# Performance work log

Hardware: AMD Instinct MI355X
Metric: run time of the kernel (lower is better)

## Reference

```python
import jax, jax.numpy as jnp
import numpy as np

N_NODES = 100000
N_EDGES = 1600000
DIM = 128
N_GRAPHS = 64
N_LAYERS = 7
LEAKY_SLOPE = 0.01
BN_EPS = 1e-5


def setup_inputs() -> dict:
    key = jax.random.key(0)
    ks = jax.random.split(key, 6)
    x = jax.random.normal(ks[0], (N_NODES, DIM), dtype=jnp.float32)
    edge_index = jax.random.randint(ks[1], (2, N_EDGES), 0, N_NODES, dtype=jnp.int64)
    batch = jnp.sort(jax.random.randint(ks[2], (N_NODES,), 0, N_GRAPHS, dtype=jnp.int64))
    # GCNConv weights (Glorot-ish scale), biases, BatchNorm affine params
    Ws = jax.random.normal(ks[3], (N_LAYERS, DIM, DIM), dtype=jnp.float32) * (1.0 / np.sqrt(DIM))
    bs = jnp.zeros((N_LAYERS, DIM), dtype=jnp.float32)
    gammas = jnp.ones((N_LAYERS, DIM), dtype=jnp.float32)
    betas = jnp.zeros((N_LAYERS, DIM), dtype=jnp.float32)
    return {"x": x, "edge_index": edge_index, "batch": batch,
            "Ws": Ws, "bs": bs, "gammas": gammas, "betas": betas}


def reference(x, edge_index, batch, Ws, bs, gammas, betas):
    N = x.shape[0]
    # Add self-loops once (shared by all 7 GCNConv layers)
    loops = jnp.arange(N, dtype=edge_index.dtype)
    src = jnp.concatenate([edge_index[0], loops])  # [E+N]
    dst = jnp.concatenate([edge_index[1], loops])  # [E+N]
    # Symmetric normalization: deg over destination (incl. self-loops)
    deg = jax.ops.segment_sum(jnp.ones_like(dst, dtype=x.dtype), dst, num_segments=N)
    dinv = jax.lax.rsqrt(jnp.maximum(deg, 1.0))  # deg >= 1 from self-loops
    norm = dinv[src] * dinv[dst]                 # [E+N]

    def block(h, W, b, gamma, beta):
        # GCNConv: linear -> gather -> normalized scatter-add
        h = h @ W + b                                            # [N, D]
        msgs = h[src] * norm[:, None]                            # [E+N, D]
        h = jax.ops.segment_sum(msgs, dst, num_segments=N)       # [N, D]
        # LeakyReLU then BatchNorm (batch statistics over nodes)
        h = jax.nn.leaky_relu(h, negative_slope=LEAKY_SLOPE)
        mu = jnp.mean(h, axis=0)
        var = jnp.mean((h - mu) ** 2, axis=0)
        h = (h - mu) * jax.lax.rsqrt(var + BN_EPS) * gamma + beta
        return h

    h = x
    for i in range(N_LAYERS):
        h = block(h, Ws[i], bs[i], gammas[i], betas[i])

    # global_mean_pool over graph ids
    sums = jax.ops.segment_sum(h, batch, num_segments=N_GRAPHS)          # [G, D]
    cnt = jax.ops.segment_sum(jnp.ones((N,), h.dtype), batch, num_segments=N_GRAPHS)
    return sums / jnp.maximum(cnt, 1.0)[:, None]
```

## Files before the change

kernel.cpp:

```cpp
#include <hip/hip_runtime.h>
#include <hip/hip_fp16.h>

#define DIMM 128
#define LEAKY_S 0.01f
#define EPS_BN 1e-5f

typedef _Float16 half8 __attribute__((ext_vector_type(8)));
typedef float f32x4 __attribute__((ext_vector_type(4)));


__global__ __launch_bounds__(256) void k_deg(const int* __restrict__ dst, int* __restrict__ deg, int E, int N) {
    int i = blockIdx.x * 256 + threadIdx.x;
    if (i < E) {
        int d = dst[i];
        if ((unsigned)d < (unsigned)N) atomicAdd(&deg[d], 1);
    }
}

__global__ __launch_bounds__(256) void k_dinv(const int* __restrict__ deg, float* __restrict__ dinv, int N) {
    int i = blockIdx.x * 256 + threadIdx.x;
    if (i < N) dinv[i] = rsqrtf((float)(deg[i] + 1));
}

__global__ __launch_bounds__(256) void k_scanA(const int* __restrict__ deg, int* __restrict__ bsum, int n) {
    __shared__ int ws[4];
    int tid = threadIdx.x, lane = tid & 63, wid = tid >> 6;
    int base = blockIdx.x * 1024;
    int s = 0;
    #pragma unroll
    for (int j = 0; j < 4; ++j) {
        int i = base + j * 256 + tid;
        if (i < n) s += deg[i];
    }
    #pragma unroll
    for (int off = 32; off > 0; off >>= 1) s += __shfl_down(s, (unsigned)off, 64);
    if (lane == 0) ws[wid] = s;
    __syncthreads();
    if (tid == 0) bsum[blockIdx.x] = ws[0] + ws[1] + ws[2] + ws[3];
}

__global__ __launch_bounds__(64) void k_scanB(const int* __restrict__ bsum, int* __restrict__ bofs,
                                              int* __restrict__ rowptr, int nb, int n) {
    if (threadIdx.x == 0) {
        int run = 0;
        for (int j = 0; j < nb; ++j) { bofs[j] = run; run += bsum[j]; }
        rowptr[n] = run;
    }
}

__global__ __launch_bounds__(1024) void k_scanC(const int* __restrict__ deg, const int* __restrict__ bofs,
                                                int* __restrict__ rowptr, int n) {
    __shared__ int wsum[16];
    int tid = threadIdx.x, lane = tid & 63, wid = tid >> 6;
    int i = blockIdx.x * 1024 + tid;
    int v = (i < n) ? deg[i] : 0;
    int s = v;
    #pragma unroll
    for (int off = 1; off < 64; off <<= 1) {
        int t = __shfl_up(s, (unsigned)off, 64);
        if (lane >= off) s += t;
    }
    if (lane == 63) wsum[wid] = s;
    __syncthreads();
    if (wid == 0 && lane < 16) {
        int ws = wsum[lane];
        #pragma unroll
        for (int off = 1; off < 16; off <<= 1) {
            int t = __shfl_up(ws, (unsigned)off, 64);
            if (lane >= off) ws += t;
        }
        wsum[lane] = ws;
    }
    __syncthreads();
    int woff = wid ? wsum[wid - 1] : 0;
    if (i < n) rowptr[i] = bofs[blockIdx.x] + woff + (s - v);
}

__global__ __launch_bounds__(256) void k_fill(const int* __restrict__ src, const int* __restrict__ dst,
                                              const int* __restrict__ rowptr, int* __restrict__ cursor,
                                              const float* __restrict__ dinv,
                                              int2* __restrict__ csr, int E, int N) {
    int i = blockIdx.x * 256 + threadIdx.x;
    if (i < E) {
        int d = dst[i], s = src[i];
        if ((unsigned)d < (unsigned)N && (unsigned)s < (unsigned)N) {
            int pos = atomicAdd(&cursor[d], 1);
            int idx = rowptr[d] + pos;
            csr[idx] = make_int2(s, __float_as_int(dinv[s] * dinv[d]));
        }
    }
}


__global__ __launch_bounds__(256) void k_wprep(const float* __restrict__ Ws, __half* __restrict__ Wt) {
    int l = blockIdx.y;
    int i = blockIdx.x * 256 + threadIdx.x;
    int n = i >> 7, k = i & 127;
    Wt[(size_t)l * DIMM * DIMM + n * DIMM + k] = __float2half(Ws[(size_t)l * DIMM * DIMM + k * DIMM + n]);
}


__global__ __launch_bounds__(256) void k_gemm(const void* __restrict__ A, const __half* __restrict__ Wt,
                                              const float* __restrict__ bias, const float* __restrict__ ss,
                                              __half* __restrict__ out, int N, int a_half) {
    __shared__ char smem[128 * 272];
    int tid = threadIdx.x;
    int lane = tid & 63, wid = tid >> 6;
    int quad = lane >> 4, lm = lane & 15;
    int row0 = blockIdx.x * 128;

    {
        int seg = tid & 31;
        int col = seg * 4;
        float4 sc = *(const float4*)(ss + col);
        float4 sh = *(const float4*)(ss + 128 + col);
        const float*  Af = (const float*)A;
        const __half* Ah = (const __half*)A;
        for (int i = tid; i < 128 * 32; i += 256) {
            int r = i >> 5;
            int gr = row0 + r;
            float4 v = make_float4(0.f, 0.f, 0.f, 0.f);
            if (gr < N) {
                if (a_half) {
                    union { uint2 u; __half2 h2[2]; } ld;
                    ld.u = *(const uint2*)(Ah + (size_t)gr * DIMM + col);
                    float2 f0 = __half22float2(ld.h2[0]);
                    float2 f1 = __half22float2(ld.h2[1]);
                    v = make_float4(f0.x, f0.y, f1.x, f1.y);
                } else {
                    v = *(const float4*)(Af + (size_t)gr * DIMM + col);
                }
                v.x = v.x * sc.x + sh.x; v.y = v.y * sc.y + sh.y;
                v.z = v.z * sc.z + sh.z; v.w = v.w * sc.w + sh.w;
            }
            union { _Float16 h[4]; uint2 u; } pk;
            pk.h[0] = (_Float16)v.x; pk.h[1] = (_Float16)v.y;
            pk.h[2] = (_Float16)v.z; pk.h[3] = (_Float16)v.w;
            *(uint2*)(smem + r * 272 + seg * 8) = pk.u;
        }
    }

    f32x4 acc[2][8];
    #pragma unroll
    for (int c = 0; c < 8; ++c) {
        float bc = bias[c * 16 + lm];
        acc[0][c] = (f32x4){bc, bc, bc, bc};
        acc[1][c] = acc[0][c];
    }
    __syncthreads();

    const _Float16* Wt16 = (const _Float16*)Wt;
    #pragma unroll
    for (int kc = 0; kc < 4; ++kc) {
        half8 a0 = *(const half8*)(smem + (wid * 32 + lm) * 272 + kc * 64 + quad * 16);
        half8 a1 = *(const half8*)(smem + (wid * 32 + 16 + lm) * 272 + kc * 64 + quad * 16);
        #pragma unroll
        for (int c = 0; c < 8; ++c) {
            half8 b = *(const half8*)(Wt16 + (c * 16 + lm) * DIMM + kc * 32 + quad * 8);
            acc[0][c] = __builtin_amdgcn_mfma_f32_16x16x32_f16(a0, b, acc[0][c], 0, 0, 0);
            acc[1][c] = __builtin_amdgcn_mfma_f32_16x16x32_f16(a1, b, acc[1][c], 0, 0, 0);
        }
    }

    __syncthreads();
    #pragma unroll
    for (int r = 0; r < 2; ++r)
        #pragma unroll
        for (int c = 0; c < 8; ++c)
            #pragma unroll
            for (int i = 0; i < 4; ++i) {
                int rit = wid * 32 + r * 16 + quad * 4 + i;
                int col = c * 16 + lm;
                *(_Float16*)(smem + rit * 256 + col * 2) = (_Float16)acc[r][c][i];
            }
    __syncthreads();
    for (int i = tid; i < 128 * 16; i += 256) {
        int r = i >> 4, seg = i & 15;
        int gr = row0 + r;
        if (gr < N)
            ((uint4*)(out + (size_t)gr * DIMM))[seg] = ((const uint4*)(smem + r * 256))[seg];
    }
}


__global__ __launch_bounds__(256) void k_agg(const __half* __restrict__ t, __half* __restrict__ out,
                                             const int* __restrict__ rowptr, const int2* __restrict__ csr,
                                             const float* __restrict__ dinv,
                                             float* __restrict__ stats, int N, int nwaves) {
    int tid = threadIdx.x;
    int lane = tid & 63, wid = tid >> 6;
    int grp = lane >> 4;
    int l16 = lane & 15;
    int gw = blockIdx.x * 4 + wid;

    float sx[8] = {0.f, 0.f, 0.f, 0.f, 0.f, 0.f, 0.f, 0.f};
    float qx[8] = {0.f, 0.f, 0.f, 0.f, 0.f, 0.f, 0.f, 0.f};

    int node = gw;
    int e0 = 0, e1 = 0;
    float di = 0.f;
    if (node < N) { e0 = rowptr[node]; e1 = rowptr[node + 1]; di = dinv[node]; }

    while (node < N) {
        int nxt = node + nwaves;
        int ep0 = 0, ep1 = 0;
        float dip = 0.f;
        if (nxt < N) { ep0 = rowptr[nxt]; ep1 = rowptr[nxt + 1]; dip = dinv[nxt]; }

        union { half8 h; __half2 h2[4]; } us;
        us.h = *(const half8*)(t + ((size_t)(unsigned)node << 7) + l16 * 8);

        float v[8] = {0.f, 0.f, 0.f, 0.f, 0.f, 0.f, 0.f, 0.f};

        for (int e = e0; e < e1; e += 32) {
            int2 c[8];
            int last = e1 - 1;
            #pragma unroll
            for (int j = 0; j < 8; ++j) {
                int idx = e + 4 * j + grp;
                int idxc = idx < last ? idx : last;
                c[j] = csr[idxc];
                if (idx >= e1) c[j].y = 0;
            }
            #pragma unroll
            for (int j = 0; j < 8; ++j) {
                float wgt = __int_as_float(c[j].y);
                union { half8 h; __half2 h2[4]; } g;
                g.h = *(const half8*)(t + ((size_t)(unsigned)c[j].x << 7) + l16 * 8);
                #pragma unroll
                for (int p = 0; p < 4; ++p) {
                    float2 f = __half22float2(g.h2[p]);
                    v[2 * p]     = fmaf(wgt, f.x, v[2 * p]);
                    v[2 * p + 1] = fmaf(wgt, f.y, v[2 * p + 1]);
                }
            }
        }

        float sn = (grp == 0) ? di * di : 0.f;
        #pragma unroll
        for (int p = 0; p < 4; ++p) {
            float2 f = __half22float2(us.h2[p]);
            v[2 * p]     = fmaf(sn, f.x, v[2 * p]);
            v[2 * p + 1] = fmaf(sn, f.y, v[2 * p + 1]);
        }

        #pragma unroll
        for (int i = 0; i < 8; ++i) {
            v[i] += __shfl_down(v[i], 32, 64);
            v[i] += __shfl_down(v[i], 16, 64);
        }
        if (grp == 0) {
            union { _Float16 h[8]; uint4 u4; } pk;
            #pragma unroll
            for (int i = 0; i < 8; ++i) {
                v[i] = v[i] > 0.f ? v[i] : LEAKY_S * v[i];
                sx[i] += v[i];
                qx[i] += v[i] * v[i];
                pk.h[i] = (_Float16)v[i];
            }
            *(uint4*)(out + ((size_t)(unsigned)node << 7) + l16 * 8) = pk.u4;
        }

        node = nxt; e0 = ep0; e1 = ep1; di = dip;
    }

    __shared__ float red[4 * 128];
    if (grp == 0) {
        *(float4*)(red + wid * 128 + l16 * 8)     = make_float4(sx[0], sx[1], sx[2], sx[3]);
        *(float4*)(red + wid * 128 + l16 * 8 + 4) = make_float4(sx[4], sx[5], sx[6], sx[7]);
    }
    __syncthreads();
    if (tid < 128) {
        float s = red[tid] + red[128 + tid] + red[256 + tid] + red[384 + tid];
        atomicAdd(&stats[tid], s);
    }
    __syncthreads();
    if (grp == 0) {
        *(float4*)(red + wid * 128 + l16 * 8)     = make_float4(qx[0], qx[1], qx[2], qx[3]);
        *(float4*)(red + wid * 128 + l16 * 8 + 4) = make_float4(qx[4], qx[5], qx[6], qx[7]);
    }
    __syncthreads();
    if (tid < 128) {
        float s = red[tid] + red[128 + tid] + red[256 + tid] + red[384 + tid];
        atomicAdd(&stats[128 + tid], s);
    }
}

__global__ __launch_bounds__(128) void k_bnfin(const float* __restrict__ stats, const float* __restrict__ gamma,
                                               const float* __restrict__ beta, float* __restrict__ ss_out,
                                               float inv_n) {
    int c = threadIdx.x;
    float mu  = stats[c] * inv_n;
    float var = stats[128 + c] * inv_n - mu * mu;
    float a = gamma[c] * rsqrtf(var + EPS_BN);
    ss_out[c]       = a;
    ss_out[128 + c] = beta[c] - mu * a;
}

__global__ __launch_bounds__(128) void k_init_ss(float* __restrict__ ss) {
    int c = threadIdx.x;
    ss[c] = 1.0f;
    ss[128 + c] = 0.0f;
}


__global__ __launch_bounds__(64) void k_cnt_bs(const int* __restrict__ batch, int* __restrict__ cnt, int N, int G) {
    int g = blockIdx.x * 64 + threadIdx.x;
    if (g >= G) return;
    int lo = 0, hi = N;
    while (lo < hi) { int mid = (lo + hi) >> 1; if (batch[mid] < g) lo = mid + 1; else hi = mid; }
    int lb = lo;
    lo = 0; hi = N;
    while (lo < hi) { int mid = (lo + hi) >> 1; if (batch[mid] <= g) lo = mid + 1; else hi = mid; }
    cnt[g] = lo - lb;
}

__global__ __launch_bounds__(128) void k_pool(const __half* __restrict__ h, const int* __restrict__ batch,
                                              float* __restrict__ pool, int N, int G) {
    const int CHUNK = 128;
    int start = blockIdx.x * CHUNK;
    if (start >= N) return;
    int end = min(start + CHUNK, N);
    int tid = threadIdx.x;
    float acc = 0.f;
    int cur = batch[start];
    for (int n = start; n < end; ++n) {
        int g = batch[n];
        if (g != cur) {
            if ((unsigned)cur < (unsigned)G) atomicAdd(&pool[(size_t)cur * DIMM + tid], acc);
            acc = 0.f; cur = g;
        }
        acc += __half2float(h[(size_t)n * DIMM + tid]);
    }
    if ((unsigned)cur < (unsigned)G) atomicAdd(&pool[(size_t)cur * DIMM + tid], acc);
}

__global__ __launch_bounds__(256) void k_poolfin(const float* __restrict__ pool, const int* __restrict__ cnt,
                                                 const float* __restrict__ ss, float* __restrict__ out, int G) {
    int idx = blockIdx.x * 256 + threadIdx.x;
    if (idx < G * DIMM) {
        int g = idx >> 7, c = idx & 127;
        float m = pool[idx] / (float)max(cnt[g], 1);
        out[idx] = ss[c] * m + ss[128 + c];
    }
}


extern "C" void kernel_launch(void* const* d_in, const int* in_sizes, int n_in,
                              void* d_out, int out_size, void* d_ws, size_t ws_size,
                              hipStream_t stream) {
    const float* x      = (const float*)d_in[0];
    const int*   ei     = (const int*)d_in[1];
    const int*   batch  = (const int*)d_in[2];
    const float* Ws     = (const float*)d_in[3];
    const float* bs     = (const float*)d_in[4];
    const float* gammas = (const float*)d_in[5];
    const float* betas  = (const float*)d_in[6];
    float* outp = (float*)d_out;

    int N = in_sizes[2];
    int E = in_sizes[1] / 2;
    int L = in_sizes[3] / (DIMM * DIMM);
    int G = out_size / DIMM;

    const int* srcv = ei;
    const int* dstv = ei + E;

    int nb = (N + 1023) / 1024;

    char* w = (char*)d_ws;
    auto alloc = [&](size_t bytes) { char* p = w; w += (bytes + 511) & ~size_t(511); return p; };
    int*    deg    = (int*)   alloc((size_t)N * 4);
    int*    cursor = (int*)   alloc((size_t)N * 4);
    int*    rowptr = (int*)   alloc((size_t)(N + 1) * 4);
    int*    bsum   = (int*)   alloc((size_t)nb * 4);
    int*    bofs   = (int*)   alloc((size_t)nb * 4);
    int2*   csr    = (int2*)  alloc((size_t)E * 8);
    float*  dinv   = (float*) alloc((size_t)N * 4);
    __half* hA     = (__half*)alloc((size_t)N * DIMM * 2);
    __half* hB     = (__half*)alloc((size_t)N * DIMM * 2);
    __half* Wt     = (__half*)alloc((size_t)L * DIMM * DIMM * 2);
    float*  stats  = (float*) alloc((size_t)L * 256 * 4);
    float*  ss     = (float*) alloc((size_t)(L + 1) * 256 * 4);
    float*  pool   = (float*) alloc((size_t)G * DIMM * 4);
    int*    cnt    = (int*)   alloc((size_t)G * 4);

    hipMemsetAsync(deg,    0, (size_t)N * 4, stream);
    hipMemsetAsync(cursor, 0, (size_t)N * 4, stream);
    hipMemsetAsync(stats,  0, (size_t)L * 256 * 4, stream);
    hipMemsetAsync(pool,   0, (size_t)G * DIMM * 4, stream);

    k_init_ss<<<1, 128, 0, stream>>>(ss);
    k_wprep<<<dim3(64, L), 256, 0, stream>>>(Ws, Wt);
    k_deg  <<<(E + 255) / 256, 256, 0, stream>>>(dstv, deg, E, N);
    k_dinv <<<(N + 255) / 256, 256, 0, stream>>>(deg, dinv, N);
    k_scanA<<<nb, 256, 0, stream>>>(deg, bsum, N);
    k_scanB<<<1, 64, 0, stream>>>(bsum, bofs, rowptr, nb, N);
    k_scanC<<<nb, 1024, 0, stream>>>(deg, bofs, rowptr, N);
    k_fill <<<(E + 255) / 256, 256, 0, stream>>>(srcv, dstv, rowptr, cursor, dinv, csr, E, N);

    const void* cur_in = (const void*)x;
    int a_half = 0;
    for (int l = 0; l < L; ++l) {
        k_gemm<<<(N + 127) / 128, 256, 0, stream>>>(cur_in, Wt + (size_t)l * DIMM * DIMM,
                                                    bs + (size_t)l * DIMM, ss + (size_t)l * 256, hA, N, a_half);
        const int nblk = 2048;
        k_agg<<<nblk, 256, 0, stream>>>(hA, hB, rowptr, csr, dinv,
                                        stats + (size_t)l * 256, N, nblk * 4);
        k_bnfin<<<1, 128, 0, stream>>>(stats + (size_t)l * 256, gammas + (size_t)l * DIMM,
                                       betas + (size_t)l * DIMM, ss + (size_t)(l + 1) * 256, 1.0f / (float)N);
        cur_in = (const void*)hB;
        a_half = 1;
    }

    k_cnt_bs<<<(G + 63) / 64, 64, 0, stream>>>(batch, cnt, N, G);
    k_pool<<<(N + 127) / 128, 128, 0, stream>>>(hB, batch, pool, N, G);
    k_poolfin<<<(G * DIMM + 255) / 256, 256, 0, stream>>>(pool, cnt, ss + (size_t)L * 256, outp, G);
}
```

Before: 1.177 ms.

## Fold BN finalize into GEMM prologue and prefetch next node's CSR edges in aggregation

Drops the separate k_bnfin and k_init_ss launches. Each GEMM block now computes the BatchNorm scale and shift from the raw stats in shared memory, and the pool-finish kernel does the same for the last layer. The aggregation kernel prefetches the first 32 CSR entries of the next node while it finishes the current one, to hide edge-list load latency. The cost is redundant BN math in every GEMM block and extra registers held across iterations of the aggregation loop.

```diff
diff --git a/kernel.cpp b/kernel.cpp
--- a/kernel.cpp
+++ b/kernel.cpp
@@ -101,19 +101,35 @@
 
 
 __global__ __launch_bounds__(256) void k_gemm(const void* __restrict__ A, const __half* __restrict__ Wt,
-                                              const float* __restrict__ bias, const float* __restrict__ ss,
-                                              __half* __restrict__ out, int N, int a_half) {
+                                              const float* __restrict__ bias,
+                                              const float* __restrict__ stats, const float* __restrict__ gamma,
+                                              const float* __restrict__ beta,
+                                              __half* __restrict__ out, int N, int a_half, float inv_n) {
     __shared__ char smem[128 * 272];
+    __shared__ float ssm[256];
     int tid = threadIdx.x;
     int lane = tid & 63, wid = tid >> 6;
     int quad = lane >> 4, lm = lane & 15;
     int row0 = blockIdx.x * 128;
 
+    if (a_half && tid < 128) {
+        float mu  = stats[tid] * inv_n;
+        float var = stats[128 + tid] * inv_n - mu * mu;
+        float a = gamma[tid] * rsqrtf(var + EPS_BN);
+        ssm[tid]       = a;
+        ssm[128 + tid] = beta[tid] - mu * a;
+    }
+    __syncthreads();
+
     {
         int seg = tid & 31;
         int col = seg * 4;
-        float4 sc = *(const float4*)(ss + col);
-        float4 sh = *(const float4*)(ss + 128 + col);
+        float4 sc = make_float4(1.f, 1.f, 1.f, 1.f);
+        float4 sh = make_float4(0.f, 0.f, 0.f, 0.f);
+        if (a_half) {
+            sc = *(const float4*)(ssm + col);
+            sh = *(const float4*)(ssm + 128 + col);
+        }
         const float*  Af = (const float*)A;
         const __half* Ah = (const __half*)A;
         for (int i = tid; i < 128 * 32; i += 256) {
@@ -126,12 +142,11 @@
                     ld.u = *(const uint2*)(Ah + (size_t)gr * DIMM + col);
                     float2 f0 = __half22float2(ld.h2[0]);
                     float2 f1 = __half22float2(ld.h2[1]);
-                    v = make_float4(f0.x, f0.y, f1.x, f1.y);
+                    v = make_float4(f0.x * sc.x + sh.x, f0.y * sc.y + sh.y,
+                                    f1.x * sc.z + sh.z, f1.y * sc.w + sh.w);
                 } else {
                     v = *(const float4*)(Af + (size_t)gr * DIMM + col);
                 }
-                v.x = v.x * sc.x + sh.x; v.y = v.y * sc.y + sh.y;
-                v.z = v.z * sc.z + sh.z; v.w = v.w * sc.w + sh.w;
             }
             union { _Float16 h[4]; uint2 u; } pk;
             pk.h[0] = (_Float16)v.x; pk.h[1] = (_Float16)v.y;
@@ -199,7 +214,20 @@
     int node = gw;
     int e0 = 0, e1 = 0;
     float di = 0.f;
-    if (node < N) { e0 = rowptr[node]; e1 = rowptr[node + 1]; di = dinv[node]; }
+    int2 c[8];
+    if (node < N) {
+        e0 = rowptr[node]; e1 = rowptr[node + 1]; di = dinv[node];
+        int last = e1 - 1;
+        #pragma unroll
+        for (int j = 0; j < 8; ++j) {
+            if (e0 + 4 * j < e1) {
+                int idx = e0 + 4 * j + grp;
+                int idxc = idx < last ? idx : last;
+                c[j] = csr[idxc];
+                if (idx >= e1) c[j].y = 0;
+            }
+        }
+    }
 
     while (node < N) {
         int nxt = node + nwaves;
@@ -212,18 +240,9 @@
 
         float v[8] = {0.f, 0.f, 0.f, 0.f, 0.f, 0.f, 0.f, 0.f};
 
-        for (int e = e0; e < e1; e += 32) {
-            int2 c[8];
-            int last = e1 - 1;
-            #pragma unroll
-            for (int j = 0; j < 8; ++j) {
-                int idx = e + 4 * j + grp;
-                int idxc = idx < last ? idx : last;
-                c[j] = csr[idxc];
-                if (idx >= e1) c[j].y = 0;
-            }
-            #pragma unroll
-            for (int j = 0; j < 8; ++j) {
+        #pragma unroll
+        for (int j = 0; j < 8; ++j) {
+            if (e0 + 4 * j < e1) {
                 float wgt = __int_as_float(c[j].y);
                 union { half8 h; __half2 h2[4]; } g;
                 g.h = *(const half8*)(t + ((size_t)(unsigned)c[j].x << 7) + l16 * 8);
@@ -235,6 +254,27 @@
                 }
             }
         }
+        for (int e = e0 + 32; e < e1; e += 32) {
+            int last = e1 - 1;
+            #pragma unroll
+            for (int j = 0; j < 8; ++j) {
+                if (e + 4 * j < e1) {
+                    int idx = e + 4 * j + grp;
+                    int idxc = idx < last ? idx : last;
+                    int2 cw = csr[idxc];
+                    if (idx >= e1) cw.y = 0;
+                    float wgt = __int_as_float(cw.y);
+                    union { half8 h; __half2 h2[4]; } g;
+                    g.h = *(const half8*)(t + ((size_t)(unsigned)cw.x << 7) + l16 * 8);
+                    #pragma unroll
+                    for (int p = 0; p < 4; ++p) {
+                        float2 f = __half22float2(g.h2[p]);
+                        v[2 * p]     = fmaf(wgt, f.x, v[2 * p]);
+                        v[2 * p + 1] = fmaf(wgt, f.y, v[2 * p + 1]);
+                    }
+                }
+            }
+        }
 
         float sn = (grp == 0) ? di * di : 0.f;
         #pragma unroll
@@ -242,6 +282,19 @@
             float2 f = __half22float2(us.h2[p]);
             v[2 * p]     = fmaf(sn, f.x, v[2 * p]);
             v[2 * p + 1] = fmaf(sn, f.y, v[2 * p + 1]);
+        }
+
+        if (nxt < N) {
+            int lastn = ep1 - 1;
+            #pragma unroll
+            for (int j = 0; j < 8; ++j) {
+                if (ep0 + 4 * j < ep1) {
+                    int idx = ep0 + 4 * j + grp;
+                    int idxc = idx < lastn ? idx : lastn;
+                    c[j] = csr[idxc];
+                    if (idx >= ep1) c[j].y = 0;
+                }
+            }
         }
 
         #pragma unroll
@@ -284,23 +337,6 @@
         float s = red[tid] + red[128 + tid] + red[256 + tid] + red[384 + tid];
         atomicAdd(&stats[128 + tid], s);
     }
-}
-
-__global__ __launch_bounds__(128) void k_bnfin(const float* __restrict__ stats, const float* __restrict__ gamma,
-                                               const float* __restrict__ beta, float* __restrict__ ss_out,
-                                               float inv_n) {
-    int c = threadIdx.x;
-    float mu  = stats[c] * inv_n;
-    float var = stats[128 + c] * inv_n - mu * mu;
-    float a = gamma[c] * rsqrtf(var + EPS_BN);
-    ss_out[c]       = a;
-    ss_out[128 + c] = beta[c] - mu * a;
-}
-
-__global__ __launch_bounds__(128) void k_init_ss(float* __restrict__ ss) {
-    int c = threadIdx.x;
-    ss[c] = 1.0f;
-    ss[128 + c] = 0.0f;
 }
 
 
@@ -336,12 +372,18 @@
 }
 
 __global__ __launch_bounds__(256) void k_poolfin(const float* __restrict__ pool, const int* __restrict__ cnt,
-                                                 const float* __restrict__ ss, float* __restrict__ out, int G) {
+                                                 const float* __restrict__ stats, const float* __restrict__ gamma,
+                                                 const float* __restrict__ beta,
+                                                 float* __restrict__ out, int G, float inv_n) {
     int idx = blockIdx.x * 256 + threadIdx.x;
     if (idx < G * DIMM) {
         int g = idx >> 7, c = idx & 127;
+        float mu  = stats[c] * inv_n;
+        float var = stats[128 + c] * inv_n - mu * mu;
+        float a = gamma[c] * rsqrtf(var + EPS_BN);
+        float b = beta[c] - mu * a;
         float m = pool[idx] / (float)max(cnt[g], 1);
-        out[idx] = ss[c] * m + ss[128 + c];
+        out[idx] = a * m + b;
     }
 }
 
@@ -381,7 +423,6 @@
     __half* hB     = (__half*)alloc((size_t)N * DIMM * 2);
     __half* Wt     = (__half*)alloc((size_t)L * DIMM * DIMM * 2);
     float*  stats  = (float*) alloc((size_t)L * 256 * 4);
-    float*  ss     = (float*) alloc((size_t)(L + 1) * 256 * 4);
     float*  pool   = (float*) alloc((size_t)G * DIMM * 4);
     int*    cnt    = (int*)   alloc((size_t)G * 4);
 
@@ -390,7 +431,8 @@
     hipMemsetAsync(stats,  0, (size_t)L * 256 * 4, stream);
     hipMemsetAsync(pool,   0, (size_t)G * DIMM * 4, stream);
 
-    k_init_ss<<<1, 128, 0, stream>>>(ss);
+    float inv_n = 1.0f / (float)N;
+
     k_wprep<<<dim3(64, L), 256, 0, stream>>>(Ws, Wt);
     k_deg  <<<(E + 255) / 256, 256, 0, stream>>>(dstv, deg, E, N);
     k_dinv <<<(N + 255) / 256, 256, 0, stream>>>(deg, dinv, N);
@@ -402,18 +444,21 @@
     const void* cur_in = (const void*)x;
     int a_half = 0;
     for (int l = 0; l < L; ++l) {
+        const float* st = (l > 0) ? stats + (size_t)(l - 1) * 256 : stats;
+        const float* gm = (l > 0) ? gammas + (size_t)(l - 1) * DIMM : gammas;
+        const float* bt = (l > 0) ? betas + (size_t)(l - 1) * DIMM : betas;
         k_gemm<<<(N + 127) / 128, 256, 0, stream>>>(cur_in, Wt + (size_t)l * DIMM * DIMM,
-                                                    bs + (size_t)l * DIMM, ss + (size_t)l * 256, hA, N, a_half);
+                                                    bs + (size_t)l * DIMM, st, gm, bt, hA, N, a_half, inv_n);
         const int nblk = 2048;
         k_agg<<<nblk, 256, 0, stream>>>(hA, hB, rowptr, csr, dinv,
                                         stats + (size_t)l * 256, N, nblk * 4);
-        k_bnfin<<<1, 128, 0, stream>>>(stats + (size_t)l * 256, gammas + (size_t)l * DIMM,
-                                       betas + (size_t)l * DIMM, ss + (size_t)(l + 1) * 256, 1.0f / (float)N);
         cur_in = (const void*)hB;
         a_half = 1;
     }
 
     k_cnt_bs<<<(G + 63) / 64, 64, 0, stream>>>(batch, cnt, N, G);
     k_pool<<<(N + 127) / 128, 128, 0, stream>>>(hB, batch, pool, N, G);
-    k_poolfin<<<(G * DIMM + 255) / 256, 256, 0, stream>>>(pool, cnt, ss + (size_t)L * 256, outp, G);
-}
+    k_poolfin<<<(G * DIMM + 255) / 256, 256, 0, stream>>>(pool, cnt, stats + (size_t)(L - 1) * 256,
+                                                          gammas + (size_t)(L - 1) * DIMM,
+                                                          betas + (size_t)(L - 1) * DIMM, outp, G, inv_n);
+}
```

After: 1.368 ms. 1.16x slower.

## Fold BatchNorm affine into GEMM weights and bias, swizzle LDS A-tile

Applied to the files above, without the earlier changes.

The BatchNorm scale and shift of the previous layer are folded into the next layer's weight matrix and bias by a new per-layer k_wbn kernel. This replaces the separate k_bnfin/k_init_ss kernels and removes the per-element FMA in the GEMM A-load. The GEMM A tile is now loaded as 16-byte fp16 chunks into an unpadded LDS layout with an XOR swizzle, which avoids bank conflicts and cuts LDS use. The trade-off is a small launch each layer and rounding of the scaled weights to fp16, which changes numerics slightly.

```diff
diff --git a/kernel.cpp b/kernel.cpp
--- a/kernel.cpp
+++ b/kernel.cpp
@@ -92,58 +92,70 @@
 }
 
 
-__global__ __launch_bounds__(256) void k_wprep(const float* __restrict__ Ws, __half* __restrict__ Wt) {
-    int l = blockIdx.y;
-    int i = blockIdx.x * 256 + threadIdx.x;
-    int n = i >> 7, k = i & 127;
-    Wt[(size_t)l * DIMM * DIMM + n * DIMM + k] = __float2half(Ws[(size_t)l * DIMM * DIMM + k * DIMM + n]);
+__global__ __launch_bounds__(128) void k_wbn(const float* __restrict__ W, const float* __restrict__ bias,
+                                             const float* __restrict__ stats, const float* __restrict__ gamma,
+                                             const float* __restrict__ beta,
+                                             __half* __restrict__ Wt, float* __restrict__ bias2,
+                                             int ident, float inv_n) {
+    __shared__ float red2[2];
+    int n = blockIdx.x;
+    int k = threadIdx.x;
+    float a = 1.f, b = 0.f;
+    if (!ident) {
+        float mu  = stats[k] * inv_n;
+        float var = stats[128 + k] * inv_n - mu * mu;
+        a = gamma[k] * rsqrtf(var + EPS_BN);
+        b = beta[k] - mu * a;
+    }
+    float w = W[k * DIMM + n];
+    Wt[n * DIMM + k] = __float2half(a * w);
+    float p = b * w;
+    #pragma unroll
+    for (int off = 32; off > 0; off >>= 1) p += __shfl_down(p, (unsigned)off, 64);
+    if ((k & 63) == 0) red2[k >> 6] = p;
+    __syncthreads();
+    if (k == 0) bias2[n] = bias[n] + red2[0] + red2[1];
 }
 
 
 __global__ __launch_bounds__(256) void k_gemm(const void* __restrict__ A, const __half* __restrict__ Wt,
-                                              const float* __restrict__ bias, const float* __restrict__ ss,
+                                              const float* __restrict__ bias2,
                                               __half* __restrict__ out, int N, int a_half) {
-    __shared__ char smem[128 * 272];
+    __shared__ char smem[128 * 256];
     int tid = threadIdx.x;
     int lane = tid & 63, wid = tid >> 6;
     int quad = lane >> 4, lm = lane & 15;
     int row0 = blockIdx.x * 128;
 
-    {
-        int seg = tid & 31;
-        int col = seg * 4;
-        float4 sc = *(const float4*)(ss + col);
-        float4 sh = *(const float4*)(ss + 128 + col);
-        const float*  Af = (const float*)A;
-        const __half* Ah = (const __half*)A;
-        for (int i = tid; i < 128 * 32; i += 256) {
-            int r = i >> 5;
-            int gr = row0 + r;
-            float4 v = make_float4(0.f, 0.f, 0.f, 0.f);
-            if (gr < N) {
-                if (a_half) {
-                    union { uint2 u; __half2 h2[2]; } ld;
-                    ld.u = *(const uint2*)(Ah + (size_t)gr * DIMM + col);
-                    float2 f0 = __half22float2(ld.h2[0]);
-                    float2 f1 = __half22float2(ld.h2[1]);
-                    v = make_float4(f0.x, f0.y, f1.x, f1.y);
-                } else {
-                    v = *(const float4*)(Af + (size_t)gr * DIMM + col);
-                }
-                v.x = v.x * sc.x + sh.x; v.y = v.y * sc.y + sh.y;
-                v.z = v.z * sc.z + sh.z; v.w = v.w * sc.w + sh.w;
+    const float*  Af = (const float*)A;
+    const __half* Ah = (const __half*)A;
+    #pragma unroll
+    for (int it = 0; it < 8; ++it) {
+        int i = it * 256 + tid;
+        int r = i >> 4, c = i & 15;
+        int gr = row0 + r;
+        union { _Float16 h[8]; uint4 u; } pk;
+        if (gr < N) {
+            if (a_half) {
+                pk.u = *(const uint4*)(Ah + (size_t)gr * DIMM + c * 8);
+            } else {
+                float4 f0 = *(const float4*)(Af + (size_t)gr * DIMM + c * 8);
+                float4 f1 = *(const float4*)(Af + (size_t)gr * DIMM + c * 8 + 4);
+                pk.h[0] = (_Float16)f0.x; pk.h[1] = (_Float16)f0.y;
+                pk.h[2] = (_Float16)f0.z; pk.h[3] = (_Float16)f0.w;
+                pk.h[4] = (_Float16)f1.x; pk.h[5] = (_Float16)f1.y;
+                pk.h[6] = (_Float16)f1.z; pk.h[7] = (_Float16)f1.w;
             }
-            union { _Float16 h[4]; uint2 u; } pk;
-            pk.h[0] = (_Float16)v.x; pk.h[1] = (_Float16)v.y;
-            pk.h[2] = (_Float16)v.z; pk.h[3] = (_Float16)v.w;
-            *(uint2*)(smem + r * 272 + seg * 8) = pk.u;
-        }
+        } else {
+            pk.u = make_uint4(0, 0, 0, 0);
+        }
+        *(uint4*)(smem + r * 256 + ((c ^ (r & 7)) << 4)) = pk.u;
     }
 
     f32x4 acc[2][8];
     #pragma unroll
     for (int c = 0; c < 8; ++c) {
-        float bc = bias[c * 16 + lm];
+        float bc = bias2[c * 16 + lm];
         acc[0][c] = (f32x4){bc, bc, bc, bc};
         acc[1][c] = acc[0][c];
     }
@@ -152,8 +164,9 @@
     const _Float16* Wt16 = (const _Float16*)Wt;
     #pragma unroll
     for (int kc = 0; kc < 4; ++kc) {
-        half8 a0 = *(const half8*)(smem + (wid * 32 + lm) * 272 + kc * 64 + quad * 16);
-        half8 a1 = *(const half8*)(smem + (wid * 32 + 16 + lm) * 272 + kc * 64 + quad * 16);
+        int sw = ((kc * 4 + quad) ^ (lm & 7)) << 4;
+        half8 a0 = *(const half8*)(smem + (wid * 32 + lm) * 256 + sw);
+        half8 a1 = *(const half8*)(smem + (wid * 32 + 16 + lm) * 256 + sw);
         #pragma unroll
         for (int c = 0; c < 8; ++c) {
             half8 b = *(const half8*)(Wt16 + (c * 16 + lm) * DIMM + kc * 32 + quad * 8);
@@ -286,23 +299,6 @@
     }
 }
 
-__global__ __launch_bounds__(128) void k_bnfin(const float* __restrict__ stats, const float* __restrict__ gamma,
-                                               const float* __restrict__ beta, float* __restrict__ ss_out,
-                                               float inv_n) {
-    int c = threadIdx.x;
-    float mu  = stats[c] * inv_n;
-    float var = stats[128 + c] * inv_n - mu * mu;
-    float a = gamma[c] * rsqrtf(var + EPS_BN);
-    ss_out[c]       = a;
-    ss_out[128 + c] = beta[c] - mu * a;
-}
-
-__global__ __launch_bounds__(128) void k_init_ss(float* __restrict__ ss) {
-    int c = threadIdx.x;
-    ss[c] = 1.0f;
-    ss[128 + c] = 0.0f;
-}
-
 
 __global__ __launch_bounds__(64) void k_cnt_bs(const int* __restrict__ batch, int* __restrict__ cnt, int N, int G) {
     int g = blockIdx.x * 64 + threadIdx.x;
@@ -336,12 +332,18 @@
 }
 
 __global__ __launch_bounds__(256) void k_poolfin(const float* __restrict__ pool, const int* __restrict__ cnt,
-                                                 const float* __restrict__ ss, float* __restrict__ out, int G) {
+                                                 const float* __restrict__ stats, const float* __restrict__ gamma,
+                                                 const float* __restrict__ beta,
+                                                 float* __restrict__ out, int G, float inv_n) {
     int idx = blockIdx.x * 256 + threadIdx.x;
     if (idx < G * DIMM) {
         int g = idx >> 7, c = idx & 127;
+        float mu  = stats[c] * inv_n;
+        float var = stats[128 + c] * inv_n - mu * mu;
+        float a = gamma[c] * rsqrtf(var + EPS_BN);
+        float b = beta[c] - mu * a;
         float m = pool[idx] / (float)max(cnt[g], 1);
-        out[idx] = ss[c] * m + ss[128 + c];
+        out[idx] = a * m + b;
     }
 }
 
@@ -379,9 +381,9 @@
     float*  dinv   = (float*) alloc((size_t)N * 4);
     __half* hA     = (__half*)alloc((size_t)N * DIMM * 2);
     __half* hB     = (__half*)alloc((size_t)N * DIMM * 2);
-    __half* Wt     = (__half*)alloc((size_t)L * DIMM * DIMM * 2);
+    __half* Wt     = (__half*)alloc((size_t)DIMM * DIMM * 2);
+    float*  bias2  = (float*) alloc((size_t)DIMM * 4);
     float*  stats  = (float*) alloc((size_t)L * 256 * 4);
-    float*  ss     = (float*) alloc((size_t)(L + 1) * 256 * 4);
     float*  pool   = (float*) alloc((size_t)G * DIMM * 4);
     int*    cnt    = (int*)   alloc((size_t)G * 4);
 
@@ -390,8 +392,8 @@
     hipMemsetAsync(stats,  0, (size_t)L * 256 * 4, stream);
     hipMemsetAsync(pool,   0, (size_t)G * DIMM * 4, stream);
 
-    k_init_ss<<<1, 128, 0, stream>>>(ss);
-    k_wprep<<<dim3(64, L), 256, 0, stream>>>(Ws, Wt);
+    float inv_n = 1.0f / (float)N;
+
     k_deg  <<<(E + 255) / 256, 256, 0, stream>>>(dstv, deg, E, N);
     k_dinv <<<(N + 255) / 256, 256, 0, stream>>>(deg, dinv, N);
     k_scanA<<<nb, 256, 0, stream>>>(deg, bsum, N);
@@ -402,18 +404,22 @@
     const void* cur_in = (const void*)x;
     int a_half = 0;
     for (int l = 0; l < L; ++l) {
-        k_gemm<<<(N + 127) / 128, 256, 0, stream>>>(cur_in, Wt + (size_t)l * DIMM * DIMM,
-                                                    bs + (size_t)l * DIMM, ss + (size_t)l * 256, hA, N, a_half);
+        const float* st = (l > 0) ? stats + (size_t)(l - 1) * 256 : stats;
+        const float* gm = (l > 0) ? gammas + (size_t)(l - 1) * DIMM : gammas;
+        const float* bt = (l > 0) ? betas + (size_t)(l - 1) * DIMM : betas;
+        k_wbn<<<DIMM, DIMM, 0, stream>>>(Ws + (size_t)l * DIMM * DIMM, bs + (size_t)l * DIMM,
+                                         st, gm, bt, Wt, bias2, (l == 0) ? 1 : 0, inv_n);
+        k_gemm<<<(N + 127) / 128, 256, 0, stream>>>(cur_in, Wt, bias2, hA, N, a_half);
         const int nblk = 2048;
         k_agg<<<nblk, 256, 0, stream>>>(hA, hB, rowptr, csr, dinv,
                                         stats + (size_t)l * 256, N, nblk * 4);
-        k_bnfin<<<1, 128, 0, stream>>>(stats + (size_t)l * 256, gammas + (size_t)l * DIMM,
-                                       betas + (size_t)l * DIMM, ss + (size_t)(l + 1) * 256, 1.0f / (float)N);
         cur_in = (const void*)hB;
         a_half = 1;
     }
 
     k_cnt_bs<<<(G + 63) / 64, 64, 0, stream>>>(batch, cnt, N, G);
     k_pool<<<(N + 127) / 128, 128, 0, stream>>>(hB, batch, pool, N, G);
-    k_poolfin<<<(G * DIMM + 255) / 256, 256, 0, stream>>>(pool, cnt, ss + (size_t)L * 256, outp, G);
-}
+    k_poolfin<<<(G * DIMM + 255) / 256, 256, 0, stream>>>(pool, cnt, stats + (size_t)(L - 1) * 256,
+                                                          gammas + (size_t)(L - 1) * DIMM,
+                                                          betas + (size_t)(L - 1) * DIMM, outp, G, inv_n);
+}
```

New measurement: 1.167 ms. About the same (-0.9%).
